# Optimization experiments

Measured on AMD Instinct MI355X. Metric: run time of the kernel, lower is better.

The kernel has to match this reference:

```python
import jax, jax.numpy as jnp
import numpy as np

K = 16
BN_EPS = 1e-3  # keras BatchNormalization default epsilon
LRELU_ALPHA = 0.1


def _lrelu(x):
    return jnp.where(x > 0, x, LRELU_ALPHA * x)


def _bn(x, gamma, beta):
    # training-mode batch norm over all axes except the last (channels)
    axes = tuple(range(x.ndim - 1))
    m = jnp.mean(x, axis=axes)
    v = jnp.var(x, axis=axes)
    return gamma * (x - m) * jax.lax.rsqrt(v + BN_EPS) + beta


def setup_inputs() -> dict:
    key = jax.random.key(0)
    ks = jax.random.split(key, 14)
    N, P, Cp, C0 = 32, 1024, 3, 64
    channels = [128, 128, 256]
    inp = {
        "points": jax.random.normal(ks[0], (N, P, Cp), dtype=jnp.float32),
        "features": jax.random.normal(ks[1], (N, P, C0), dtype=jnp.float32),
    }
    # edge-conv 1x1 weights (no bias, with_bn=True); glorot-ish scaling
    c_in = 2 * C0
    for i, c_out in enumerate(channels):
        scale = (2.0 / (c_in + c_out)) ** 0.5
        inp[f"W{i}"] = jax.random.normal(ks[2 + i], (c_in, c_out), dtype=jnp.float32) * scale
        inp[f"g{i}"] = jnp.ones((c_out,), dtype=jnp.float32)
        inp[f"b{i}"] = jnp.zeros((c_out,), dtype=jnp.float32)
        c_in = c_out
    # shortcut 1x1 conv C0 -> channels[-1]
    scale = (2.0 / (C0 + channels[-1])) ** 0.5
    inp["Wsc"] = jax.random.normal(ks[10], (C0, channels[-1]), dtype=jnp.float32) * scale
    inp["gsc"] = jnp.ones((channels[-1],), dtype=jnp.float32)
    inp["bsc"] = jnp.zeros((channels[-1],), dtype=jnp.float32)
    return inp


def reference(points, features, W0, g0, b0, W1, g1, b1, W2, g2, b2, Wsc, gsc, bsc):
    # pairwise squared distance matrix D: (N, P, P)
    r = jnp.sum(points * points, axis=-1)
    D = r[:, :, None] - 2.0 * jnp.einsum("npc,nqc->npq", points, points) + r[:, None, :]
    # kNN indices, excluding self (first neighbor)
    _, idx = jax.lax.top_k(-D, K + 1)
    idx = idx[:, :, 1:]  # (N, P, K)
    # gather neighbor features per batch element -> (N, P, K, C0)
    knn_fts = jax.vmap(lambda f, i: f[i])(features, idx)
    center = jnp.broadcast_to(features[:, :, None, :], knn_fts.shape)
    x = jnp.concatenate([center, knn_fts - center], axis=-1)  # (N, P, K, 2*C0)
    for W, g, b in ((W0, g0, b0), (W1, g1, b1), (W2, g2, b2)):
        x = _lrelu(_bn(jnp.einsum("npkc,cd->npkd", x, W), g, b))
    fts = jnp.mean(x, axis=2)  # average pooling over K -> (N, P, C_out)
    sc = _bn(jnp.einsum("npc,cd->npd", features, Wsc), gsc, bsc)
    return _lrelu(sc + fts)
```

## Files before the change

### kernel.cpp

```cpp
#include <hip/hip_runtime.h>
#include <stdint.h>

typedef __bf16 bf16x8 __attribute__((ext_vector_type(8)));
typedef float f32x4 __attribute__((ext_vector_type(4)));

union FragU { uint4 q; bf16x8 v; };

__device__ __forceinline__ float bf2f(uint32_t h){
  union U{uint32_t u; float f;} x; x.u = h<<16; return x.f;
}
__device__ __forceinline__ uint32_t f2bf(float f){
  union U{float f; uint32_t u;} x; x.f=f;
  return (x.u + 0x7FFFu + ((x.u>>16)&1u)) >> 16;
}
__device__ __forceinline__ float lrelu(float x){ return fmaxf(x, 0.1f*x); }

__global__ __launch_bounds__(256) void knn_kernel(const float* __restrict__ points, int* __restrict__ idx){
  __shared__ float sx[1024], sy[1024], sz[1024];
  __shared__ unsigned long long scand[4][64];
  const int n = blockIdx.y;
  const float* P = points + (size_t)n*1024*3;
  for(int q=threadIdx.x; q<1024; q+=256){
    sx[q]=P[q*3+0]; sy[q]=P[q*3+1]; sz[q]=P[q*3+2];
  }
  __syncthreads();
  const int wv = threadIdx.x>>6;
  const int lane = threadIdx.x & 63;
  const int p = blockIdx.x*4 + wv;
  const double px=sx[p], py=sy[p], pz=sz[p];
  const double rp = px*px+py*py+pz*pz;
  unsigned long long e[16];
  const int prel = p - lane;
  #pragma unroll
  for(int j=0;j<16;j++){
    const int q = lane + j*64;
    double qx=sx[q], qy=sy[q], qz=sz[q];
    double rq = qx*qx+qy*qy+qz*qz;
    double dot = px*qx+py*qy+pz*qz;
    float key = fmaxf((float)((rp+rq) - 2.0*dot), 0.0f);
    if(prel == j*64) key = __builtin_inff();
    e[j] = ((unsigned long long)__float_as_uint(key) << 10) | (unsigned)q;
  }
  unsigned long long h = e[0];
  #pragma unroll
  for(int j=1;j<16;j++) h = (e[j] < h) ? e[j] : h;
  {
    unsigned long long hs = h;
    #pragma unroll
    for(int k=2;k<=64;k<<=1){
      #pragma unroll
      for(int j=32;j>0;j>>=1){
        if(j < k){
          unsigned long long o = __shfl_xor(hs, j);
          const bool keepMax = (((lane & j)!=0) ^ ((lane & k)!=0));
          hs = keepMax ? (hs > o ? hs : o) : (hs < o ? hs : o);
        }
      }
    }
    h = hs;
  }
  const unsigned long long H = __shfl(h, 15);
  int cnt = 0;
  #pragma unroll
  for(int j=0;j<16;j++) cnt += (e[j] <= H) ? 1 : 0;
  int inc = cnt;
  #pragma unroll
  for(int d=1; d<64; d<<=1){
    int t = __shfl_up(inc, d);
    if(lane >= d) inc += t;
  }
  const int m = __shfl(inc, 63);
  const int base = inc - cnt;
  int* op = idx + ((size_t)n*1024 + p)*16;
  if(m <= 64){
    unsigned long long* sc = scand[wv];
    int slot = base;
    #pragma unroll
    for(int j=0;j<16;j++){
      if(e[j] <= H){ sc[slot] = e[j]; slot++; }
    }
    unsigned long long v = (lane < m) ? sc[lane] : ~0ULL;
    #pragma unroll
    for(int k=2;k<=64;k<<=1){
      #pragma unroll
      for(int j=32;j>0;j>>=1){
        if(j < k){
          unsigned long long o = __shfl_xor(v, j);
          const bool keepMax = (((lane & j)!=0) ^ ((lane & k)!=0));
          v = keepMax ? (v > o ? v : o) : (v < o ? v : o);
        }
      }
    }
    if(lane < 16) op[lane] = (int)(v & 1023u);
  } else {
    for(int it=0; it<16; ++it){
      unsigned long long bd = e[0];
      #pragma unroll
      for(int j=1;j<16;j++) bd = (e[j] < bd) ? e[j] : bd;
      unsigned long long pk = bd;
      #pragma unroll
      for(int s=1;s<64;s<<=1){
        unsigned long long o = __shfl_xor(pk, s);
        pk = (o < pk) ? o : pk;
      }
      #pragma unroll
      for(int j=0;j<16;j++) e[j] = (e[j]==pk) ? ~0ULL : e[j];
      if(lane==0) op[it] = (int)(pk & 1023u);
    }
  }
}

__global__ void wprep_kernel(const float* __restrict__ W0, const float* __restrict__ Wsc,
                             const float* __restrict__ W1, const float* __restrict__ W2,
                             uint16_t* __restrict__ Wpp, uint16_t* __restrict__ W1p,
                             uint16_t* __restrict__ W2p){
  const int stride = gridDim.x*blockDim.x;
  const int t0 = blockIdx.x*blockDim.x + threadIdx.x;
  for(int o=t0; o<32768; o+=stride){
    int j=o&7, l=(o>>3)&63, kc=(o>>9)&1, ct=(o>>10)&3, w=o>>12;
    int k = kc*32 + (l>>4)*8 + j;
    int c = w*64 + ct*16 + (l&15);
    float val;
    if(c<128)      val = W0[k*128+c] - W0[(k+64)*128+c];
    else if(c<256) val = W0[(k+64)*128 + (c-128)];
    else           val = Wsc[k*256 + (c-256)];
    Wpp[o] = (uint16_t)f2bf(val);
  }
  for(int o=t0; o<16384; o+=stride){
    int j=o&7, l=(o>>3)&63, kc=(o>>9)&3, ct=(o>>11)&1, w=o>>12;
    int k = kc*32 + (l>>4)*8 + j, c = w*32 + ct*16 + (l&15);
    W1p[o] = (uint16_t)f2bf(W1[k*128+c]);
  }
  for(int o=t0; o<32768; o+=stride){
    int j=o&7, l=(o>>3)&63, kc=(o>>9)&3, ct=(o>>11)&3, w=o>>13;
    int k = kc*32 + (l>>4)*8 + j, c = w*64 + ct*16 + (l&15);
    W2p[o] = (uint16_t)f2bf(W2[k*256+c]);
  }
}

__global__ __launch_bounds__(512) void proj_kernel(const float* __restrict__ feat,
    const uint16_t* __restrict__ Wpp,
    float* __restrict__ F1, float* __restrict__ F2, float* __restrict__ Fsc,
    float* __restrict__ screps){
  __shared__ alignas(16) uint16_t sA[64*64];
  const int b = blockIdx.x;
  const int tid = threadIdx.x;
  {
    const int row = tid>>3, cc = tid&7;
    const float* src = feat + ((size_t)b*64+row)*64 + cc*8;
    const float4 f0 = *(const float4*)(src);
    const float4 f1 = *(const float4*)(src+4);
    uint32_t pk[4] = { f2bf(f0.x)|(f2bf(f0.y)<<16), f2bf(f0.z)|(f2bf(f0.w)<<16),
                       f2bf(f1.x)|(f2bf(f1.y)<<16), f2bf(f1.z)|(f2bf(f1.w)<<16) };
    int bo = row*128 + cc*16; bo ^= (row&7)<<4;
    *(uint4*)((char*)sA + bo) = make_uint4(pk[0],pk[1],pk[2],pk[3]);
  }
  __syncthreads();
  const int w = tid>>6, l = tid&63;
  FragU bfr[4][2];
  #pragma unroll
  for(int ct=0;ct<4;ct++)
    #pragma unroll
    for(int kc=0;kc<2;kc++)
      bfr[ct][kc].q = *(const uint4*)(Wpp + ((size_t)((w*4+ct)*2+kc))*512 + l*8);
  f32x4 acc[4][4] = {};
  #pragma unroll
  for(int rt=0;rt<4;rt++){
    FragU a[2];
    #pragma unroll
    for(int kc=0;kc<2;kc++){
      const int row = rt*16 + (l&15);
      int bo = row*128 + kc*64 + (l>>4)*16; bo ^= (row&7)<<4;
      a[kc].q = *(const uint4*)((const char*)sA + bo);
    }
    #pragma unroll
    for(int ct=0;ct<4;ct++)
      #pragma unroll
      for(int kc=0;kc<2;kc++)
        acc[rt][ct] = __builtin_amdgcn_mfma_f32_16x16x32_bf16(a[kc].v, bfr[ct][kc].v, acc[rt][ct], 0,0,0);
  }
  #pragma unroll
  for(int rt=0;rt<4;rt++){
    #pragma unroll
    for(int ct=0;ct<4;ct++){
      const int c = w*64 + ct*16 + (l&15);
      const int rowg = b*64 + rt*16 + (l>>4)*4;
      #pragma unroll
      for(int reg=0;reg<4;reg++){
        float v = acc[rt][ct][reg];
        if(c < 128)      F1[(size_t)(rowg+reg)*128 + c] = v;
        else if(c < 256) F2[(size_t)(rowg+reg)*128 + (c-128)] = v;
        else             Fsc[(size_t)(rowg+reg)*256 + (c-256)] = v;
      }
    }
  }
  if(w>=4){
    #pragma unroll
    for(int ct=0;ct<4;ct++){
      float s=0.f, sq=0.f;
      #pragma unroll
      for(int rt=0;rt<4;rt++)
        #pragma unroll
        for(int reg=0;reg<4;reg++){ float v=acc[rt][ct][reg]; s+=v; sq+=v*v; }
      s += __shfl_xor(s,16); sq += __shfl_xor(sq,16);
      s += __shfl_xor(s,32); sq += __shfl_xor(sq,32);
      if(l<16){
        const int c = (w-4)*64 + ct*16 + l;
        atomicAdd(&screps[((b&31)*2+0)*256 + c], s);
        atomicAdd(&screps[((b&31)*2+1)*256 + c], sq);
      }
    }
  }
}

__global__ __launch_bounds__(256) void y0stats_kernel(const float* __restrict__ F1,
    const float* __restrict__ F2, const int* __restrict__ idx, float* __restrict__ reps){
  __shared__ int sIdx[256];
  const int tid = threadIdx.x;
  const int r0 = blockIdx.x*256;
  sIdx[tid] = idx[r0 + tid];
  __syncthreads();
  const int cg = tid & 31;
  const int rs = tid >> 5;
  const int nbase = (r0 >> 14) << 10;
  f32x4 s = {0,0,0,0}, sq = {0,0,0,0};
  for(int rr=0; rr<32; rr+=4){
    #pragma unroll
    for(int u=0;u<4;u++){
      const int r = rs*32 + rr + u;
      const int np = (r0 + r) >> 4;
      const int g = sIdx[r];
      const float4 a = *(const float4*)(F1 + (size_t)np*128 + cg*4);
      const float4 c = *(const float4*)(F2 + (size_t)(nbase + g)*128 + cg*4);
      float v0=a.x+c.x, v1=a.y+c.y, v2=a.z+c.z, v3=a.w+c.w;
      s[0]+=v0; s[1]+=v1; s[2]+=v2; s[3]+=v3;
      sq[0]+=v0*v0; sq[1]+=v1*v1; sq[2]+=v2*v2; sq[3]+=v3*v3;
    }
  }
  #pragma unroll
  for(int e=0;e<4;e++){
    s[e]  += __shfl_xor(s[e], 32);
    sq[e] += __shfl_xor(sq[e], 32);
  }
  if((tid&63) < 32){
    const int rep = blockIdx.x & 31;
    #pragma unroll
    for(int e=0;e<4;e++){
      atomicAdd(&reps[(rep*2+0)*128 + cg*4+e], s[e]);
      atomicAdd(&reps[(rep*2+1)*128 + cg*4+e], sq[e]);
    }
  }
}

__global__ void finalize_kernel(const float* __restrict__ reps, const float* __restrict__ gamma,
    const float* __restrict__ beta, float* __restrict__ s, float* __restrict__ t,
    int C, float inv_cnt){
  int c = threadIdx.x;
  if(c>=C) return;
  float sum=0.f, sq=0.f;
  for(int r2=0;r2<32;r2++){ sum += reps[(r2*2+0)*C + c]; sq += reps[(r2*2+1)*C + c]; }
  float m = sum*inv_cnt;
  float var = sq*inv_cnt - m*m;
  float sc = gamma[c]*rsqrtf(var + 1e-3f);
  s[c]=sc; t[c]=beta[c] - m*sc;
}

__global__ __launch_bounds__(256) void layer1_kernel(
    const float* __restrict__ F1, const float* __restrict__ F2, const int* __restrict__ idx,
    const uint16_t* __restrict__ W1p, const float* __restrict__ s0, const float* __restrict__ t0,
    uint16_t* __restrict__ y1, float* __restrict__ reps1){
  __shared__ alignas(16) uint16_t sA[64*128];
  __shared__ int sIdx[64];
  const int b = blockIdx.x;
  const int tid = threadIdx.x;
  if(tid < 64) sIdx[tid] = idx[b*64 + tid];
  const int row0 = tid>>4, q = tid&15;
  const float4 sc0a = *(const float4*)(s0 + q*8);
  const float4 sc0b = *(const float4*)(s0 + q*8 + 4);
  const float4 tt0a = *(const float4*)(t0 + q*8);
  const float4 tt0b = *(const float4*)(t0 + q*8 + 4);
  const int wv = tid>>6, l = tid&63;
  FragU bfr[2][4];
  #pragma unroll
  for(int ct=0;ct<2;ct++)
    #pragma unroll
    for(int kc=0;kc<4;kc++)
      bfr[ct][kc].q = *(const uint4*)(W1p + ((size_t)((wv*2+ct)*4+kc))*512 + l*8);
  __syncthreads();
  {
    const int npb = b*4;
    const int nbase = (b >> 8) << 10;
    int gg[4];
    #pragma unroll
    for(int jj=0;jj<4;jj++) gg[jj] = sIdx[row0 + jj*16];
    float4 va[4][4];
    #pragma unroll
    for(int jj=0;jj<4;jj++){
      const int np = npb + jj;
      const float* pf1 = F1 + (size_t)np*128 + q*8;
      const float* pf2 = F2 + (size_t)(nbase + gg[jj])*128 + q*8;
      va[jj][0] = *(const float4*)(pf1);
      va[jj][1] = *(const float4*)(pf1+4);
      va[jj][2] = *(const float4*)(pf2);
      va[jj][3] = *(const float4*)(pf2+4);
    }
    #pragma unroll
    for(int jj=0;jj<4;jj++){
      const int rw = row0 + jj*16;
      float v[8] = {va[jj][0].x+va[jj][2].x, va[jj][0].y+va[jj][2].y,
                    va[jj][0].z+va[jj][2].z, va[jj][0].w+va[jj][2].w,
                    va[jj][1].x+va[jj][3].x, va[jj][1].y+va[jj][3].y,
                    va[jj][1].z+va[jj][3].z, va[jj][1].w+va[jj][3].w};
      const float sc[8] = {sc0a.x,sc0a.y,sc0a.z,sc0a.w, sc0b.x,sc0b.y,sc0b.z,sc0b.w};
      const float tt[8] = {tt0a.x,tt0a.y,tt0a.z,tt0a.w, tt0b.x,tt0b.y,tt0b.z,tt0b.w};
      uint32_t pk[4];
      #pragma unroll
      for(int e=0;e<4;e++){
        float x0 = lrelu(sc[e*2]*v[e*2] + tt[e*2]);
        float x1 = lrelu(sc[e*2+1]*v[e*2+1] + tt[e*2+1]);
        pk[e] = f2bf(x0) | (f2bf(x1)<<16);
      }
      int bo = rw*256 + q*16; bo ^= (rw&7)<<4;
      *(uint4*)((char*)sA + bo) = make_uint4(pk[0],pk[1],pk[2],pk[3]);
    }
  }
  __syncthreads();
  f32x4 acc[4][2] = {};
  #pragma unroll
  for(int rt=0;rt<4;rt++){
    FragU a[4];
    #pragma unroll
    for(int kc=0;kc<4;kc++){
      const int rw = rt*16 + (l&15);
      int bo = rw*256 + kc*64 + (l>>4)*16; bo ^= (rw&7)<<4;
      a[kc].q = *(const uint4*)((const char*)sA + bo);
    }
    #pragma unroll
    for(int ct=0;ct<2;ct++)
      #pragma unroll
      for(int kc=0;kc<4;kc++)
        acc[rt][ct] = __builtin_amdgcn_mfma_f32_16x16x32_bf16(a[kc].v, bfr[ct][kc].v, acc[rt][ct], 0,0,0);
  }
  float ss[2]={0.f,0.f}, sq[2]={0.f,0.f};
  #pragma unroll
  for(int rt=0;rt<4;rt++)
    #pragma unroll
    for(int ct=0;ct<2;ct++)
      #pragma unroll
      for(int reg=0;reg<4;reg++){
        float v = acc[rt][ct][reg];
        ss[ct]+=v; sq[ct]+=v*v;
        const int CI = ((rt*4+wv)*2+ct)*4+reg;
        y1[(size_t)b*8192 + CI*64 + l] = (uint16_t)f2bf(v);
      }
  #pragma unroll
  for(int ct=0;ct<2;ct++){
    float a=ss[ct], b2=sq[ct];
    a += __shfl_xor(a,16); b2 += __shfl_xor(b2,16);
    a += __shfl_xor(a,32); b2 += __shfl_xor(b2,32);
    if((l>>4)==0){
      const int c = wv*32 + ct*16 + l;
      atomicAdd(&reps1[((b&31)*2+0)*128 + c], a);
      atomicAdd(&reps1[((b&31)*2+1)*128 + c], b2);
    }
  }
}

template<int FINAL>
__global__ __launch_bounds__(256, 2) void layer2_kernel(
    const uint16_t* __restrict__ y1, const uint16_t* __restrict__ W2p,
    const float* __restrict__ s1, const float* __restrict__ t1,
    float* __restrict__ reps2,
    const float* __restrict__ s2, const float* __restrict__ t2,
    const float* __restrict__ Fsc, const float* __restrict__ ssc, const float* __restrict__ tsc,
    float* __restrict__ out){
  __shared__ alignas(16) uint16_t sA[2][8192];
  __shared__ float sBN[256];
  const int tid = threadIdx.x;
  const int wv = tid>>6, l = tid&63;
  if(tid<128){ sBN[tid]=s1[tid]; sBN[128+tid]=t1[tid]; }
  FragU bfr[4][4];
  #pragma unroll
  for(int ct=0;ct<4;ct++)
    #pragma unroll
    for(int kc=0;kc<4;kc++)
      bfr[ct][kc].q = *(const uint4*)(W2p + ((size_t)((wv*4+ct)*4+kc))*512 + l*8);
  int uc0[4], ubo[4];
  #pragma unroll
  for(int k=0;k<4;k++){
    const int u = tid + k*256;
    const int l8 = u&7, CI = u>>3;
    const int reg = CI&3, ct = (CI>>2)&1, w = (CI>>3)&3, rt = CI>>5;
    const int row = rt*16 + (l8>>1)*4 + reg;
    const int c0 = w*32 + ct*16 + (l8&1)*8;
    uc0[k] = c0;
    ubo[k] = (row*256 + c0*2) ^ ((row&7)<<4);
  }
  float sc2v[4], tt2v[4], sscv[4], tscv[4];
  if(FINAL){
    #pragma unroll
    for(int ct=0;ct<4;ct++){
      const int c = wv*64 + ct*16 + (l&15);
      sc2v[ct]=s2[c]; tt2v[ct]=t2[c]; sscv[ct]=ssc[c]; tscv[ct]=tsc[c];
    }
  }
  const int bt0 = blockIdx.x*16;
  uint4 va[4];
  #pragma unroll
  for(int k=0;k<4;k++)
    va[k] = *(const uint4*)(y1 + (size_t)bt0*8192 + (size_t)(tid+k*256)*8);
  __syncthreads();
  #pragma unroll
  for(int k=0;k<4;k++){
    const float4 sa = *(const float4*)(&sBN[uc0[k]]);
    const float4 sb = *(const float4*)(&sBN[uc0[k]+4]);
    const float4 ta = *(const float4*)(&sBN[128+uc0[k]]);
    const float4 tb = *(const float4*)(&sBN[128+uc0[k]+4]);
    const float scv[8]={sa.x,sa.y,sa.z,sa.w, sb.x,sb.y,sb.z,sb.w};
    const float ttv[8]={ta.x,ta.y,ta.z,ta.w, tb.x,tb.y,tb.z,tb.w};
    const uint32_t e[4] = {va[k].x, va[k].y, va[k].z, va[k].w};
    uint32_t pk[4];
    #pragma unroll
    for(int j=0;j<4;j++){
      float x0 = lrelu(scv[j*2]*bf2f(e[j]&0xffffu) + ttv[j*2]);
      float x1 = lrelu(scv[j*2+1]*bf2f(e[j]>>16) + ttv[j*2+1]);
      pk[j] = f2bf(x0) | (f2bf(x1)<<16);
    }
    *(uint4*)((char*)sA[0] + ubo[k]) = make_uint4(pk[0],pk[1],pk[2],pk[3]);
  }
  __syncthreads();
  float ssA[4]={0,0,0,0}, sqA[4]={0,0,0,0};
  for(int t=0; t<16; ++t){
    const int bt = bt0 + t;
    const int p = t&1;
    if(t<15){
      #pragma unroll
      for(int k=0;k<4;k++)
        va[k] = *(const uint4*)(y1 + (size_t)(bt+1)*8192 + (size_t)(tid+k*256)*8);
    }
    f32x4 acc[4][4] = {};
    #pragma unroll
    for(int rt=0;rt<4;rt++){
      FragU a[4];
      #pragma unroll
      for(int kc=0;kc<4;kc++){
        const int rw = rt*16 + (l&15);
        int bo = rw*256 + kc*64 + (l>>4)*16; bo ^= (rw&7)<<4;
        a[kc].q = *(const uint4*)((const char*)sA[p] + bo);
      }
      #pragma unroll
      for(int ct=0;ct<4;ct++)
        #pragma unroll
        for(int kc=0;kc<4;kc++)
          acc[rt][ct] = __builtin_amdgcn_mfma_f32_16x16x32_bf16(a[kc].v, bfr[ct][kc].v, acc[rt][ct], 0,0,0);
    }
    if(FINAL==0){
      #pragma unroll
      for(int ct=0;ct<4;ct++)
        #pragma unroll
        for(int rt=0;rt<4;rt++)
          #pragma unroll
          for(int reg=0;reg<4;reg++){
            float v = acc[rt][ct][reg];
            ssA[ct]+=v; sqA[ct]+=v*v;
          }
    } else {
      #pragma unroll
      for(int rt=0;rt<4;rt++){
        const int np = bt*4 + rt;
        #pragma unroll
        for(int ct=0;ct<4;ct++){
          const int c = wv*64 + ct*16 + (l&15);
          float s=0.f;
          #pragma unroll
          for(int reg=0;reg<4;reg++) s += lrelu(sc2v[ct]*acc[rt][ct][reg] + tt2v[ct]);
          s += __shfl_xor(s,16);
          s += __shfl_xor(s,32);
          if((l>>4)==0){
            float fts = s*(1.0f/16.0f);
            float sc = sscv[ct]*Fsc[(size_t)np*256+c] + tscv[ct];
            out[(size_t)np*256+c] = lrelu(sc + fts);
          }
        }
      }
    }
    if(t<15){
      #pragma unroll
      for(int k=0;k<4;k++){
        const float4 sa = *(const float4*)(&sBN[uc0[k]]);
        const float4 sb = *(const float4*)(&sBN[uc0[k]+4]);
        const float4 ta = *(const float4*)(&sBN[128+uc0[k]]);
        const float4 tb = *(const float4*)(&sBN[128+uc0[k]+4]);
        const float scv[8]={sa.x,sa.y,sa.z,sa.w, sb.x,sb.y,sb.z,sb.w};
        const float ttv[8]={ta.x,ta.y,ta.z,ta.w, tb.x,tb.y,tb.z,tb.w};
        const uint32_t e[4] = {va[k].x, va[k].y, va[k].z, va[k].w};
        uint32_t pk[4];
        #pragma unroll
        for(int j=0;j<4;j++){
          float x0 = lrelu(scv[j*2]*bf2f(e[j]&0xffffu) + ttv[j*2]);
          float x1 = lrelu(scv[j*2+1]*bf2f(e[j]>>16) + ttv[j*2+1]);
          pk[j] = f2bf(x0) | (f2bf(x1)<<16);
        }
        *(uint4*)((char*)sA[p^1] + ubo[k]) = make_uint4(pk[0],pk[1],pk[2],pk[3]);
      }
    }
    __syncthreads();
  }
  if(FINAL==0){
    #pragma unroll
    for(int ct=0;ct<4;ct++){
      float a=ssA[ct], b2=sqA[ct];
      a += __shfl_xor(a,16); b2 += __shfl_xor(b2,16);
      a += __shfl_xor(a,32); b2 += __shfl_xor(b2,32);
      if((l>>4)==0){
        const int c = wv*64 + ct*16 + l;
        const int rep = blockIdx.x & 31;
        atomicAdd(&reps2[(rep*2+0)*256 + c], a);
        atomicAdd(&reps2[(rep*2+1)*256 + c], b2);
      }
    }
  }
}

extern "C" void kernel_launch(void* const* d_in, const int* in_sizes, int n_in,
                              void* d_out, int out_size, void* d_ws, size_t ws_size,
                              hipStream_t stream) {
  const float* points   = (const float*)d_in[0];
  const float* features = (const float*)d_in[1];
  const float* W0  = (const float*)d_in[2];
  const float* g0  = (const float*)d_in[3];
  const float* b0  = (const float*)d_in[4];
  const float* W1  = (const float*)d_in[5];
  const float* g1  = (const float*)d_in[6];
  const float* b1  = (const float*)d_in[7];
  const float* W2  = (const float*)d_in[8];
  const float* g2  = (const float*)d_in[9];
  const float* b2  = (const float*)d_in[10];
  const float* Wsc = (const float*)d_in[11];
  const float* gsc = (const float*)d_in[12];
  const float* bsc = (const float*)d_in[13];
  float* out = (float*)d_out;

  float* ws = (float*)d_ws;
  size_t off = 0;
  float* screps = ws + off; off += 16384;
  float* reps0  = ws + off; off += 8192;
  float* reps1  = ws + off; off += 8192;
  float* reps2  = ws + off; off += 16384;
  float* ssc = ws + off; off += 256;
  float* tsc = ws + off; off += 256;
  float* s0  = ws + off; off += 128;
  float* t0  = ws + off; off += 128;
  float* s1v = ws + off; off += 128;
  float* t1v = ws + off; off += 128;
  float* s2v = ws + off; off += 256;
  float* t2v = ws + off; off += 256;
  int*   idxb = (int*)(ws + off); off += 524288;
  float* F1  = ws + off; off += (size_t)32768*128;
  float* F2  = ws + off; off += (size_t)32768*128;
  float* Fsc = ws + off; off += (size_t)32768*256;
  uint16_t* W1p = (uint16_t*)(ws + off); off += 8192;
  uint16_t* W2p = (uint16_t*)(ws + off); off += 16384;
  uint16_t* Wpp = (uint16_t*)(ws + off); off += 16384;
  uint16_t* y1  = (uint16_t*)(ws + off); off += (size_t)33554432;

  hipMemsetAsync(d_ws, 0, 49152*sizeof(float), stream);

  knn_kernel<<<dim3(256,32), 256, 0, stream>>>(points, idxb);
  wprep_kernel<<<128, 256, 0, stream>>>(W0, Wsc, W1, W2, Wpp, W1p, W2p);
  proj_kernel<<<512, 512, 0, stream>>>(features, Wpp, F1, F2, Fsc, screps);
  finalize_kernel<<<1, 256, 0, stream>>>(screps, gsc, bsc, ssc, tsc, 256, 1.0f/32768.0f);
  y0stats_kernel<<<2048, 256, 0, stream>>>(F1, F2, idxb, reps0);
  finalize_kernel<<<1, 128, 0, stream>>>(reps0, g0, b0, s0, t0, 128, 1.0f/524288.0f);
  layer1_kernel<<<8192, 256, 0, stream>>>(F1, F2, idxb, W1p, s0, t0, y1, reps1);
  finalize_kernel<<<1, 128, 0, stream>>>(reps1, g1, b1, s1v, t1v, 128, 1.0f/524288.0f);
  layer2_kernel<0><<<512, 256, 0, stream>>>(y1, W2p, s1v, t1v, reps2,
                                            nullptr, nullptr, nullptr, nullptr, nullptr, nullptr);
  finalize_kernel<<<1, 256, 0, stream>>>(reps2, g2, b2, s2v, t2v, 256, 1.0f/524288.0f);
  layer2_kernel<1><<<512, 256, 0, stream>>>(y1, W2p, s1v, t1v, nullptr,
                                            s2v, t2v, Fsc, ssc, tsc, out);
}
```

Measured before the change: 330.2 us.

## Compute layer-2 BN statistics via Gram matrix of activations instead of full GEMM

Replaces the stats-only pass of layer 2 (a full 128->256 GEMM over all edges to get per-channel sum and sum of squares) with a Gram matrix X^T X (128x128) plus column sums of the BN1+LReLU activations, reduced across blocks. The layer-2 mean and variance are then derived algebraically as w^T colsum and w^T G w per output channel. This halves the output width of the stats GEMM and drops the atomics, but adds partial-buffer writes, a reduction kernel and an extra small kernel, and reads W2 in fp32 while activations are bf16, which may shift numerics slightly.

```diff
diff --git a/kernel.cpp b/kernel.cpp
--- a/kernel.cpp
+++ b/kernel.cpp
@@ -366,11 +366,146 @@
   }
 }
 
-template<int FINAL>
-__global__ __launch_bounds__(256, 2) void layer2_kernel(
+__global__ __launch_bounds__(256) void gram_kernel(
+    const uint16_t* __restrict__ y1, const float* __restrict__ s1, const float* __restrict__ t1,
+    float* __restrict__ Gpart, float* __restrict__ colpart){
+  __shared__ alignas(16) uint16_t sG[128*64];
+  __shared__ float sBN[256];
+  __shared__ float scol[128];
+  const int tid = threadIdx.x;
+  const int wv = tid>>6, l = tid&63;
+  if(tid<128){ sBN[tid]=s1[tid]; sBN[128+tid]=t1[tid]; }
+  int uc0[4], urow[4];
+  #pragma unroll
+  for(int k=0;k<4;k++){
+    const int u = tid + k*256;
+    const int l8=u&7, CI=u>>3;
+    const int reg=CI&3, ct=(CI>>2)&1, w8=(CI>>3)&3, rt=CI>>5;
+    urow[k] = rt*16 + (l8>>1)*4 + reg;
+    uc0[k]  = w8*32 + ct*16 + (l8&1)*8;
+  }
+  const int bt0 = blockIdx.x*16;
+  const int cch = tid & 127, rhalf = tid>>7;
+  f32x4 acc[2][8] = {};
+  float colacc = 0.f;
+  uint4 va[4];
+  #pragma unroll
+  for(int k=0;k<4;k++)
+    va[k] = *(const uint4*)(y1 + (size_t)bt0*8192 + (size_t)(tid+k*256)*8);
+  __syncthreads();
+  for(int t=0; t<16; ++t){
+    #pragma unroll
+    for(int k=0;k<4;k++){
+      const int c0 = uc0[k], row = urow[k];
+      const uint32_t e[4] = {va[k].x,va[k].y,va[k].z,va[k].w};
+      #pragma unroll
+      for(int j=0;j<4;j++){
+        const int c = c0 + 2*j;
+        float x0 = lrelu(sBN[c]*bf2f(e[j]&0xffffu) + sBN[128+c]);
+        float x1 = lrelu(sBN[c+1]*bf2f(e[j]>>16) + sBN[128+c+1]);
+        *(uint16_t*)((char*)sG + (size_t)c*128     + ((row*2) ^ ((2*j  )<<4))) = (uint16_t)f2bf(x0);
+        *(uint16_t*)((char*)sG + (size_t)(c+1)*128 + ((row*2) ^ ((2*j+1)<<4))) = (uint16_t)f2bf(x1);
+      }
+    }
+    if(t<15){
+      #pragma unroll
+      for(int k=0;k<4;k++)
+        va[k] = *(const uint4*)(y1 + (size_t)(bt0+t+1)*8192 + (size_t)(tid+k*256)*8);
+    }
+    __syncthreads();
+    #pragma unroll
+    for(int kc=0; kc<2; ++kc){
+      const int r0 = kc*32 + (l>>4)*8;
+      const int lch0 = wv*16 + (l&15);
+      const int lch1 = (wv+4)*16 + (l&15);
+      FragU fa0, fa1;
+      fa0.q = *(const uint4*)((const char*)sG + (size_t)lch0*128 + ((r0*2) ^ ((lch0&7)<<4)));
+      fa1.q = *(const uint4*)((const char*)sG + (size_t)lch1*128 + ((r0*2) ^ ((lch1&7)<<4)));
+      #pragma unroll
+      for(int gj=0; gj<8; ++gj){
+        const int bch = gj*16 + (l&15);
+        FragU fb;
+        fb.q = *(const uint4*)((const char*)sG + (size_t)bch*128 + ((r0*2) ^ ((bch&7)<<4)));
+        acc[0][gj] = __builtin_amdgcn_mfma_f32_16x16x32_bf16(fa0.v, fb.v, acc[0][gj], 0,0,0);
+        acc[1][gj] = __builtin_amdgcn_mfma_f32_16x16x32_bf16(fa1.v, fb.v, acc[1][gj], 0,0,0);
+      }
+    }
+    #pragma unroll
+    for(int s=0;s<4;s++){
+      const int r0 = rhalf*32 + s*8;
+      uint4 qv = *(const uint4*)((const char*)sG + (size_t)cch*128 + ((r0*2) ^ ((cch&7)<<4)));
+      const uint32_t ee[4]={qv.x,qv.y,qv.z,qv.w};
+      #pragma unroll
+      for(int j2=0;j2<4;j2++)
+        colacc += bf2f(ee[j2]&0xffffu) + bf2f(ee[j2]>>16);
+    }
+    __syncthreads();
+  }
+  float* gp = Gpart + (size_t)blockIdx.x*16384;
+  #pragma unroll
+  for(int gi2=0; gi2<2; ++gi2){
+    const int i0 = (wv + gi2*4)*16 + (l>>4)*4;
+    #pragma unroll
+    for(int gj=0; gj<8; ++gj){
+      const int j0 = gj*16 + (l&15);
+      #pragma unroll
+      for(int reg=0; reg<4; ++reg)
+        gp[(size_t)(i0+reg)*128 + j0] = acc[gi2][gj][reg];
+    }
+  }
+  if(tid < 128) scol[tid] = colacc;
+  __syncthreads();
+  if(tid >= 128) scol[tid-128] += colacc;
+  __syncthreads();
+  if(tid < 128) colpart[blockIdx.x*128 + tid] = scol[tid];
+}
+
+__global__ void greduce_kernel(const float* __restrict__ Gpart, const float* __restrict__ colpart,
+                               float* __restrict__ Gred, float* __restrict__ colred){
+  const int e = blockIdx.x*256 + threadIdx.x;
+  if(e < 16384){
+    float s=0.f;
+    for(int b=0;b<512;b++) s += Gpart[(size_t)b*16384 + e];
+    Gred[e]=s;
+  }
+  if(e < 128){
+    float s=0.f;
+    for(int b=0;b<512;b++) s += colpart[b*128 + e];
+    colred[e]=s;
+  }
+}
+
+__global__ void finalize2_kernel(const float* __restrict__ Gred, const float* __restrict__ colred,
+    const float* __restrict__ W2, const float* __restrict__ g2, const float* __restrict__ b2,
+    float* __restrict__ s2, float* __restrict__ t2){
+  __shared__ float wcol[128];
+  __shared__ float rr[4];
+  const int c = blockIdx.x, i = threadIdx.x;
+  wcol[i] = W2[i*256 + c];
+  __syncthreads();
+  float u = 0.f;
+  #pragma unroll 4
+  for(int ii=0; ii<128; ++ii)
+    u += Gred[ii*128 + i] * wcol[ii];
+  float v1 = wcol[i]*u;
+  float v2 = colred[i]*wcol[i];
+  #pragma unroll
+  for(int s=1;s<64;s<<=1){ v1 += __shfl_xor(v1,s); v2 += __shfl_xor(v2,s); }
+  if((i&63)==0){ rr[(i>>6)*2]=v1; rr[(i>>6)*2+1]=v2; }
+  __syncthreads();
+  if(i==0){
+    float sumsq = rr[0]+rr[2], sum = rr[1]+rr[3];
+    const float invR = 1.0f/524288.0f;
+    float mean = sum*invR;
+    float var = sumsq*invR - mean*mean;
+    float sc = g2[c]*rsqrtf(var + 1e-3f);
+    s2[c]=sc; t2[c]=b2[c]-mean*sc;
+  }
+}
+
+__global__ __launch_bounds__(256, 2) void layer2f_kernel(
     const uint16_t* __restrict__ y1, const uint16_t* __restrict__ W2p,
     const float* __restrict__ s1, const float* __restrict__ t1,
-    float* __restrict__ reps2,
     const float* __restrict__ s2, const float* __restrict__ t2,
     const float* __restrict__ Fsc, const float* __restrict__ ssc, const float* __restrict__ tsc,
     float* __restrict__ out){
@@ -397,12 +532,10 @@
     ubo[k] = (row*256 + c0*2) ^ ((row&7)<<4);
   }
   float sc2v[4], tt2v[4], sscv[4], tscv[4];
-  if(FINAL){
-    #pragma unroll
-    for(int ct=0;ct<4;ct++){
-      const int c = wv*64 + ct*16 + (l&15);
-      sc2v[ct]=s2[c]; tt2v[ct]=t2[c]; sscv[ct]=ssc[c]; tscv[ct]=tsc[c];
-    }
+  #pragma unroll
+  for(int ct=0;ct<4;ct++){
+    const int c = wv*64 + ct*16 + (l&15);
+    sc2v[ct]=s2[c]; tt2v[ct]=t2[c]; sscv[ct]=ssc[c]; tscv[ct]=tsc[c];
   }
   const int bt0 = blockIdx.x*16;
   uint4 va[4];
@@ -429,7 +562,6 @@
     *(uint4*)((char*)sA[0] + ubo[k]) = make_uint4(pk[0],pk[1],pk[2],pk[3]);
   }
   __syncthreads();
-  float ssA[4]={0,0,0,0}, sqA[4]={0,0,0,0};
   for(int t=0; t<16; ++t){
     const int bt = bt0 + t;
     const int p = t&1;
@@ -454,33 +586,21 @@
         for(int kc=0;kc<4;kc++)
           acc[rt][ct] = __builtin_amdgcn_mfma_f32_16x16x32_bf16(a[kc].v, bfr[ct][kc].v, acc[rt][ct], 0,0,0);
     }
-    if(FINAL==0){
-      #pragma unroll
-      for(int ct=0;ct<4;ct++)
+    #pragma unroll
+    for(int rt=0;rt<4;rt++){
+      const int np = bt*4 + rt;
+      #pragma unroll
+      for(int ct=0;ct<4;ct++){
+        const int c = wv*64 + ct*16 + (l&15);
+        float s=0.f;
         #pragma unroll
-        for(int rt=0;rt<4;rt++)
-          #pragma unroll
-          for(int reg=0;reg<4;reg++){
-            float v = acc[rt][ct][reg];
-            ssA[ct]+=v; sqA[ct]+=v*v;
-          }
-    } else {
-      #pragma unroll
-      for(int rt=0;rt<4;rt++){
-        const int np = bt*4 + rt;
-        #pragma unroll
-        for(int ct=0;ct<4;ct++){
-          const int c = wv*64 + ct*16 + (l&15);
-          float s=0.f;
-          #pragma unroll
-          for(int reg=0;reg<4;reg++) s += lrelu(sc2v[ct]*acc[rt][ct][reg] + tt2v[ct]);
-          s += __shfl_xor(s,16);
-          s += __shfl_xor(s,32);
-          if((l>>4)==0){
-            float fts = s*(1.0f/16.0f);
-            float sc = sscv[ct]*Fsc[(size_t)np*256+c] + tscv[ct];
-            out[(size_t)np*256+c] = lrelu(sc + fts);
-          }
+        for(int reg=0;reg<4;reg++) s += lrelu(sc2v[ct]*acc[rt][ct][reg] + tt2v[ct]);
+        s += __shfl_xor(s,16);
+        s += __shfl_xor(s,32);
+        if((l>>4)==0){
+          float fts = s*(1.0f/16.0f);
+          float sc = sscv[ct]*Fsc[(size_t)np*256+c] + tscv[ct];
+          out[(size_t)np*256+c] = lrelu(sc + fts);
         }
       }
     }
@@ -505,20 +625,6 @@
       }
     }
     __syncthreads();
-  }
-  if(FINAL==0){
-    #pragma unroll
-    for(int ct=0;ct<4;ct++){
-      float a=ssA[ct], b2=sqA[ct];
-      a += __shfl_xor(a,16); b2 += __shfl_xor(b2,16);
-      a += __shfl_xor(a,32); b2 += __shfl_xor(b2,32);
-      if((l>>4)==0){
-        const int c = wv*64 + ct*16 + l;
-        const int rep = blockIdx.x & 31;
-        atomicAdd(&reps2[(rep*2+0)*256 + c], a);
-        atomicAdd(&reps2[(rep*2+1)*256 + c], b2);
-      }
-    }
   }
 }
 
@@ -564,6 +670,11 @@
   uint16_t* Wpp = (uint16_t*)(ws + off); off += 16384;
   uint16_t* y1  = (uint16_t*)(ws + off); off += (size_t)33554432;
 
+  float* Gpart   = F1;
+  float* colpart = (float*)idxb;
+  float* Gred    = reps2;
+  float* colred  = reps1;
+
   hipMemsetAsync(d_ws, 0, 49152*sizeof(float), stream);
 
   knn_kernel<<<dim3(256,32), 256, 0, stream>>>(points, idxb);
@@ -574,9 +685,9 @@
   finalize_kernel<<<1, 128, 0, stream>>>(reps0, g0, b0, s0, t0, 128, 1.0f/524288.0f);
   layer1_kernel<<<8192, 256, 0, stream>>>(F1, F2, idxb, W1p, s0, t0, y1, reps1);
   finalize_kernel<<<1, 128, 0, stream>>>(reps1, g1, b1, s1v, t1v, 128, 1.0f/524288.0f);
-  layer2_kernel<0><<<512, 256, 0, stream>>>(y1, W2p, s1v, t1v, reps2,
-                                            nullptr, nullptr, nullptr, nullptr, nullptr, nullptr);
-  finalize_kernel<<<1, 256, 0, stream>>>(reps2, g2, b2, s2v, t2v, 256, 1.0f/524288.0f);
-  layer2_kernel<1><<<512, 256, 0, stream>>>(y1, W2p, s1v, t1v, nullptr,
-                                            s2v, t2v, Fsc, ssc, tsc, out);
-}
+  gram_kernel<<<512, 256, 0, stream>>>(y1, s1v, t1v, Gpart, colpart);
+  greduce_kernel<<<64, 256, 0, stream>>>(Gpart, colpart, Gred, colred);
+  finalize2_kernel<<<256, 128, 0, stream>>>(Gred, colred, W2, g2, b2, s2v, t2v);
+  layer2f_kernel<<<512, 256, 0, stream>>>(y1, W2p, s1v, t1v,
+                                          s2v, t2v, Fsc, ssc, tsc, out);
+}
```

Measured after the change: 363.0 us. 9.9% more time.
